# Kernel tuning notes

Hardware: AMD Instinct MI355X
Metric: run time of the kernel (lower is better)

## Reference

```python
import jax, jax.numpy as jnp
import numpy as np

B, S, D, H = 2, 2048, 1024, 16
DK = D // H  # 64


def setup_inputs() -> dict:
    key = jax.random.key(0)
    ks = jax.random.split(key, 12)
    inp = {
        "query": jax.random.normal(ks[0], (B, S, D), jnp.float32),
        "key": jax.random.normal(ks[1], (B, S, D), jnp.float32),
        "value": jax.random.normal(ks[2], (B, S, D), jnp.float32),
        "mask": jnp.ones((B, 1, S, S), jnp.float32),  # 1.0 = attend
    }
    sc = 1.0 / np.sqrt(D)
    inp["wq"] = jax.random.normal(ks[3], (D, D), jnp.float32) * sc
    inp["bq"] = jax.random.normal(ks[4], (D,), jnp.float32) * 0.01
    inp["wk"] = jax.random.normal(ks[5], (D, D), jnp.float32) * sc
    inp["bk"] = jax.random.normal(ks[6], (D,), jnp.float32) * 0.01
    inp["wv"] = jax.random.normal(ks[7], (D, D), jnp.float32) * sc
    inp["bv"] = jax.random.normal(ks[8], (D,), jnp.float32) * 0.01
    inp["wo"] = jax.random.normal(ks[9], (D, D), jnp.float32) * sc
    inp["bo"] = jax.random.normal(ks[10], (D,), jnp.float32) * 0.01
    return inp


def _split_heads(x):
    # [B, S, D] -> [B, H, S, DK]
    b, s, _ = x.shape
    return x.reshape(b, s, H, DK).transpose(0, 2, 1, 3)


def reference(query, key, value, mask, wq, bq, wk, bk, wv, bv, wo, bo):
    # Linear projections (torch Linear: x @ W.T + b)
    q = _split_heads(query @ wq.T + bq)   # [B,H,Sq,DK]
    k = _split_heads(key @ wk.T + bk)     # [B,H,Sk,DK]
    v = _split_heads(value @ wv.T + bv)   # [B,H,Sk,DK]

    attn = jnp.einsum('bhqd,bhkd->bhqk', q, k) / jnp.sqrt(jnp.float32(DK))
    # mask: 1.0 attend, 0.0 masked -> add finfo.min at masked positions
    inv = (1.0 - mask) * jnp.finfo(attn.dtype).min
    attn = attn + inv
    attention_weights = jax.nn.softmax(attn, axis=-1)  # [B,H,Sq,Sk]
    # dropout=0.0 (eval mode): identity
    ctx = jnp.einsum('bhqk,bhkd->bhqd', attention_weights, v)  # [B,H,Sq,DK]
    concat = ctx.transpose(0, 2, 1, 3).reshape(ctx.shape[0], ctx.shape[2], D)
    output = concat @ wo.T + bo
    return (output, attention_weights)
```

## Files before the change

kernel.cpp:

```cpp
#include <hip/hip_runtime.h>
#include <cstdint>

typedef short bf16x8 __attribute__((ext_vector_type(8)));
typedef float f32x4 __attribute__((ext_vector_type(4)));

#define NEG_MAX 3.402823466e38f

__device__ __forceinline__ unsigned short f2bf(float f) {
  uint32_t u = __builtin_bit_cast(uint32_t, f);
  u += 0x7FFFu + ((u >> 16) & 1u);
  return (unsigned short)(u >> 16);
}

__device__ __forceinline__ bf16x8 pack8(float4 x, float4 y) {
  bf16x8 r;
  r[0] = (short)f2bf(x.x); r[1] = (short)f2bf(x.y); r[2] = (short)f2bf(x.z); r[3] = (short)f2bf(x.w);
  r[4] = (short)f2bf(y.x); r[5] = (short)f2bf(y.y); r[6] = (short)f2bf(y.z); r[7] = (short)f2bf(y.w);
  return r;
}

__global__ __launch_bounds__(256) void cvt_w(const float* __restrict__ wq, const float* __restrict__ wk,
                                             const float* __restrict__ wv, const float* __restrict__ wo,
                                             unsigned short* __restrict__ out) {
  int i = blockIdx.x * 256 + threadIdx.x;
  const int sel = i >> 18;
  const int idx = i & 0x3FFFF;
  const float* src = (sel == 0) ? wq : (sel == 1) ? wk : (sel == 2) ? wv : wo;
  float4 v = reinterpret_cast<const float4*>(src)[idx];
  ushort4 o;
  o.x = f2bf(v.x); o.y = f2bf(v.y); o.z = f2bf(v.z); o.w = f2bf(v.w);
  reinterpret_cast<ushort4*>(out)[i] = o;
}

__global__ __launch_bounds__(256) void mask_scan(const float* __restrict__ mask,
                                                 int* __restrict__ flags) {
  const int blk = blockIdx.x;
  const int kt = blk & 31, qt = (blk >> 5) & 31, b = blk >> 10;
  const float* base = mask + ((size_t)b * 2048 + qt * 64) * 2048 + kt * 64;
  const int t = threadIdx.x;
  const int row = t >> 2, c0 = (t & 3) * 16;
  const float4* p = reinterpret_cast<const float4*>(base + (size_t)row * 2048 + c0);
  bool ones = true;
#pragma unroll
  for (int i = 0; i < 4; ++i) {
    float4 v = p[i];
    ones = ones && (v.x == 1.f) && (v.y == 1.f) && (v.z == 1.f) && (v.w == 1.f);
  }
  unsigned long long ball = __ballot(ones);
  __shared__ int sf[4];
  if ((t & 63) == 0) sf[t >> 6] = (ball == ~0ull) ? 1 : 0;
  __syncthreads();
  if (t == 0) flags[blk] = sf[0] & sf[1] & sf[2] & sf[3];
}

__global__ __launch_bounds__(256) void gemm_qkv(const float* __restrict__ Aq,
                                                const float* __restrict__ Ak,
                                                const float* __restrict__ Av,
                                                const unsigned short* __restrict__ W3,
                                                const float* __restrict__ bq,
                                                const float* __restrict__ bk,
                                                const float* __restrict__ bv,
                                                unsigned short* __restrict__ Qbf,
                                                unsigned short* __restrict__ Kbf,
                                                unsigned short* __restrict__ Vtb) {
  constexpr int KD = 1024;
  __shared__ __align__(16) unsigned short Al[128 * 32];
  __shared__ __align__(16) unsigned short Bl[128 * 32];
  const int tid = threadIdx.x;
  const int l = tid & 63;
  const int w = tid >> 6;
  const int lr = l & 15;
  const int lg = l >> 4;
  const int gm = blockIdx.y;
  const int gn = blockIdx.x;
  const int z = blockIdx.z;
  const int wr = w >> 1;
  const int wc = w & 1;

  const float* Af = (z == 0) ? Aq : (z == 1) ? Ak : Av;
  const float* bias = (z == 0) ? bq : (z == 1) ? bk : bv;
  const unsigned short* Bw = W3 + (size_t)z * 1048576;
  unsigned short* Cb = (z == 0) ? Qbf : (z == 1) ? Kbf : Vtb;

  f32x4 acc[4][4];
#pragma unroll
  for (int m = 0; m < 4; ++m)
#pragma unroll
    for (int n = 0; n < 4; ++n) acc[m][n] = (f32x4){0.f, 0.f, 0.f, 0.f};

  const int c0 = w * 2;
  const int srow = (l >> 2);
  const int scol = (l & 3) * 8;
  const unsigned short* gB = Bw + (size_t)(gn * 128) * KD;

  const int arow = tid >> 1;
  const int ahalf = tid & 1;
  const float* gA = Af + (size_t)(gm * 128 + arow) * KD + ahalf * 16;

  float4 ap[4];
  {
    const float4* p = reinterpret_cast<const float4*>(gA);
#pragma unroll
    for (int i = 0; i < 4; ++i) ap[i] = p[i];
  }

  for (int kt = 0; kt < 32; ++kt) {
    const int k0 = kt * 32;
    const unsigned short* b0 = gB + (size_t)(c0 * 16 + srow) * KD + k0 + scol;
    const unsigned short* b1 = b0 + (size_t)16 * KD;
    __builtin_amdgcn_global_load_lds((const __attribute__((address_space(1))) void*)b0,
                                     (__attribute__((address_space(3))) void*)&Bl[c0 * 512], 16, 0, 0);
    __builtin_amdgcn_global_load_lds((const __attribute__((address_space(1))) void*)b1,
                                     (__attribute__((address_space(3))) void*)&Bl[c0 * 512 + 512], 16, 0, 0);
    {
      bf16x8* dst = reinterpret_cast<bf16x8*>(&Al[arow * 32 + ahalf * 16]);
      dst[0] = pack8(ap[0], ap[1]);
      dst[1] = pack8(ap[2], ap[3]);
    }
    __syncthreads();
    if (kt + 1 < 32) {
      const float4* p = reinterpret_cast<const float4*>(gA + (kt + 1) * 32);
#pragma unroll
      for (int i = 0; i < 4; ++i) ap[i] = p[i];
    }
    bf16x8 af[4], bfr[4];
#pragma unroll
    for (int m = 0; m < 4; ++m)
      af[m] = *reinterpret_cast<const bf16x8*>(&Al[(wr * 64 + m * 16 + lr) * 32 + lg * 8]);
#pragma unroll
    for (int n = 0; n < 4; ++n)
      bfr[n] = *reinterpret_cast<const bf16x8*>(&Bl[(wc * 64 + n * 16 + lr) * 32 + lg * 8]);
#pragma unroll
    for (int m = 0; m < 4; ++m)
#pragma unroll
      for (int n = 0; n < 4; ++n)
        acc[m][n] = __builtin_amdgcn_mfma_f32_16x16x32_bf16(af[m], bfr[n], acc[m][n], 0, 0, 0);
    __syncthreads();
  }

#pragma unroll
  for (int m = 0; m < 4; ++m) {
#pragma unroll
    for (int n = 0; n < 4; ++n) {
      const int colg = gn * 128 + wc * 64 + n * 16 + lr;
      const float bv2 = bias[colg];
#pragma unroll
      for (int r = 0; r < 4; ++r) {
        const int rowg = gm * 128 + wr * 64 + m * 16 + lg * 4 + r;
        const float v = acc[m][n][r] + bv2;
        const int bb = rowg >> 11, ss = rowg & 2047;
        const int hh = colg >> 6, dk = colg & 63;
        if (z < 2)
          Cb[(((size_t)bb * 16 + hh) * 2048 + ss) * 64 + dk] = f2bf(v);
        else
          Cb[(((size_t)bb * 16 + hh) * 32 + (ss >> 6)) * 4096 + (size_t)dk * 64 + (ss & 63)] = f2bf(v);
      }
    }
  }
}

__global__ __launch_bounds__(256) void gemm_out(const unsigned short* __restrict__ A,
                                                const unsigned short* __restrict__ Bw,
                                                const float* __restrict__ bias,
                                                float* __restrict__ Cf) {
  constexpr int KD = 1024;
  __shared__ __align__(16) unsigned short Al[128 * 32];
  __shared__ __align__(16) unsigned short Bl[128 * 32];
  const int tid = threadIdx.x;
  const int l = tid & 63;
  const int w = tid >> 6;
  const int lr = l & 15;
  const int lg = l >> 4;
  const int gm = blockIdx.y;
  const int gn = blockIdx.x;
  const int wr = w >> 1;
  const int wc = w & 1;

  f32x4 acc[4][4];
#pragma unroll
  for (int m = 0; m < 4; ++m)
#pragma unroll
    for (int n = 0; n < 4; ++n) acc[m][n] = (f32x4){0.f, 0.f, 0.f, 0.f};

  const int c0 = w * 2;
  const int srow = (l >> 2);
  const int scol = (l & 3) * 8;
  const unsigned short* gA = A + (size_t)(gm * 128) * KD;
  const unsigned short* gB = Bw + (size_t)(gn * 128) * KD;

  for (int kt = 0; kt < 32; ++kt) {
    const int k0 = kt * 32;
    const unsigned short* a0 = gA + (size_t)(c0 * 16 + srow) * KD + k0 + scol;
    const unsigned short* a1 = a0 + (size_t)16 * KD;
    const unsigned short* b0 = gB + (size_t)(c0 * 16 + srow) * KD + k0 + scol;
    const unsigned short* b1 = b0 + (size_t)16 * KD;
    __builtin_amdgcn_global_load_lds((const __attribute__((address_space(1))) void*)a0,
                                     (__attribute__((address_space(3))) void*)&Al[c0 * 512], 16, 0, 0);
    __builtin_amdgcn_global_load_lds((const __attribute__((address_space(1))) void*)a1,
                                     (__attribute__((address_space(3))) void*)&Al[c0 * 512 + 512], 16, 0, 0);
    __builtin_amdgcn_global_load_lds((const __attribute__((address_space(1))) void*)b0,
                                     (__attribute__((address_space(3))) void*)&Bl[c0 * 512], 16, 0, 0);
    __builtin_amdgcn_global_load_lds((const __attribute__((address_space(1))) void*)b1,
                                     (__attribute__((address_space(3))) void*)&Bl[c0 * 512 + 512], 16, 0, 0);
    __syncthreads();
    bf16x8 af[4], bfr[4];
#pragma unroll
    for (int m = 0; m < 4; ++m)
      af[m] = *reinterpret_cast<const bf16x8*>(&Al[(wr * 64 + m * 16 + lr) * 32 + lg * 8]);
#pragma unroll
    for (int n = 0; n < 4; ++n)
      bfr[n] = *reinterpret_cast<const bf16x8*>(&Bl[(wc * 64 + n * 16 + lr) * 32 + lg * 8]);
#pragma unroll
    for (int m = 0; m < 4; ++m)
#pragma unroll
      for (int n = 0; n < 4; ++n)
        acc[m][n] = __builtin_amdgcn_mfma_f32_16x16x32_bf16(af[m], bfr[n], acc[m][n], 0, 0, 0);
    __syncthreads();
  }

#pragma unroll
  for (int m = 0; m < 4; ++m) {
#pragma unroll
    for (int n = 0; n < 4; ++n) {
      const int colg = gn * 128 + wc * 64 + n * 16 + lr;
      const float bv = bias[colg];
#pragma unroll
      for (int r = 0; r < 4; ++r) {
        const int rowg = gm * 128 + wr * 64 + m * 16 + lg * 4 + r;
        Cf[(size_t)rowg * 1024 + colg] = acc[m][n][r] + bv;
      }
    }
  }
}

__global__ __launch_bounds__(512, 4) void attn_fused(const unsigned short* __restrict__ Q,
                                                     const unsigned short* __restrict__ Kb,
                                                     const unsigned short* __restrict__ Vt,
                                                     const float* __restrict__ mask,
                                                     const int* __restrict__ flags,
                                                     float* __restrict__ wout,
                                                     unsigned short* __restrict__ ctx) {
  const int tid = threadIdx.x;
  const int l = tid & 63;
  const int w = tid >> 6;
  const int lr = l & 15;
  const int lg = l >> 4;

  const int d = blockIdx.x;
  const int bh = (d >> 7) * 8 + (d & 7);
  const int qp = (d >> 3) & 15;
  const int b = bh >> 4, h = bh & 15;
  const int q0 = qp * 128;

  __shared__ __align__(16) unsigned short KV[4][4096];
  __shared__ __align__(16) unsigned short Wl[8][16][64];

  const size_t qoff = ((size_t)bh * 2048 + (q0 + w * 16 + lr)) * 64 + lg * 8;
  const bf16x8 qf0 = *reinterpret_cast<const bf16x8*>(Q + qoff);
  const bf16x8 qf1 = *reinterpret_cast<const bf16x8*>(Q + qoff + 32);

  const int seg = tid;
  const int rs = seg >> 3, cx = (seg & 7) ^ (rs & 7);
  const unsigned short* kB = Kb + (size_t)bh * 131072;
  const unsigned short* vB = Vt + (size_t)bh * 131072;
  const size_t tS = (size_t)rs * 64 + cx * 8;
  const int ldsOff = w * 512;

  const int sA = (lg ^ (lr & 7)) << 3;
  const int sBo = ((4 + lg) ^ (lr & 7)) << 3;

  const int fbase = (b * 32 + qp * 2 + (w >> 2)) * 32;
  const uint32_t fmask = (uint32_t)__ballot(flags[fbase + (l & 31)] != 0);

  const float* mbase = mask + (size_t)b * 2048 * 2048;

#define STAGE(base_, kt_, slot_)                                                                       \
  do {                                                                                                 \
    __builtin_amdgcn_global_load_lds(                                                                  \
        (const __attribute__((address_space(1))) void*)((base_) + (size_t)(kt_) * 4096 + tS),          \
        (__attribute__((address_space(3))) void*)(&KV[slot_][0] + ldsOff), 16, 0, 0);                  \
  } while (0)

  float s0[4] = {0.f, 0.f, 0.f, 0.f};

  STAGE(kB, 0, 0);
  STAGE(kB, 1, 1);
  for (int kt = 0; kt < 32; ++kt) {
    if (kt < 31) {
      asm volatile("s_waitcnt vmcnt(1)" ::: "memory");
    } else {
      asm volatile("s_waitcnt vmcnt(0)" ::: "memory");
    }
    __builtin_amdgcn_s_barrier();
    __builtin_amdgcn_sched_barrier(0);
    const unsigned short* Ks = &KV[kt % 3][0];
    bf16x8 kf0[4], kf1[4];
#pragma unroll
    for (int n = 0; n < 4; ++n) {
      const int rb = (n * 16 + lr) * 64;
      kf0[n] = *reinterpret_cast<const bf16x8*>(&Ks[rb + sA]);
      kf1[n] = *reinterpret_cast<const bf16x8*>(&Ks[rb + sBo]);
    }
    if (kt + 2 < 32) STAGE(kB, kt + 2, (kt + 2) % 3);
    f32x4 acc[4];
#pragma unroll
    for (int n = 0; n < 4; ++n) {
      acc[n] = (f32x4){0.f, 0.f, 0.f, 0.f};
      acc[n] = __builtin_amdgcn_mfma_f32_16x16x32_bf16(qf0, kf0[n], acc[n], 0, 0, 0);
      acc[n] = __builtin_amdgcn_mfma_f32_16x16x32_bf16(qf1, kf1[n], acc[n], 0, 0, 0);
    }
    if ((fmask >> kt) & 1) {
#pragma unroll
      for (int r = 0; r < 4; ++r)
        s0[r] += __expf(acc[0][r] * 0.125f) + __expf(acc[1][r] * 0.125f) +
                 __expf(acc[2][r] * 0.125f) + __expf(acc[3][r] * 0.125f);
    } else {
#pragma unroll
      for (int r = 0; r < 4; ++r) {
        const int qrow = q0 + w * 16 + lg * 4 + r;
        const float* mp = mbase + (size_t)qrow * 2048 + kt * 64;
        float ps = 0.f;
#pragma unroll
        for (int n = 0; n < 4; ++n) {
          const float mv = mp[n * 16 + lr];
          ps += __expf(acc[n][r] * 0.125f + (1.0f - mv) * (-NEG_MAX));
        }
        s0[r] += ps;
      }
    }
  }

  float inv_s[4];
#pragma unroll
  for (int r = 0; r < 4; ++r) {
#pragma unroll
    for (int dd = 1; dd < 16; dd <<= 1) s0[r] += __shfl_xor(s0[r], dd);
    inv_s[r] = 1.0f / s0[r];
  }

  f32x4 cacc[4];
#pragma unroll
  for (int n = 0; n < 4; ++n) cacc[n] = (f32x4){0.f, 0.f, 0.f, 0.f};

  STAGE(kB, 0, 0);
  STAGE(vB, 0, 2);
  for (int kt = 0; kt < 32; ++kt) {
    const int cur = kt & 1;
    asm volatile("s_waitcnt vmcnt(0)" ::: "memory");
    __builtin_amdgcn_s_barrier();
    __builtin_amdgcn_sched_barrier(0);
    const unsigned short* Ks = &KV[cur][0];
    const unsigned short* Vs = &KV[2 + cur][0];
    bf16x8 kf0[4], kf1[4];
#pragma unroll
    for (int n = 0; n < 4; ++n) {
      const int rb = (n * 16 + lr) * 64;
      kf0[n] = *reinterpret_cast<const bf16x8*>(&Ks[rb + sA]);
      kf1[n] = *reinterpret_cast<const bf16x8*>(&Ks[rb + sBo]);
    }
    if (kt + 1 < 32) {
      STAGE(kB, kt + 1, cur ^ 1);
      STAGE(vB, kt + 1, 2 + (cur ^ 1));
    }
    f32x4 acc[4];
#pragma unroll
    for (int n = 0; n < 4; ++n) {
      acc[n] = (f32x4){0.f, 0.f, 0.f, 0.f};
      acc[n] = __builtin_amdgcn_mfma_f32_16x16x32_bf16(qf0, kf0[n], acc[n], 0, 0, 0);
      acc[n] = __builtin_amdgcn_mfma_f32_16x16x32_bf16(qf1, kf1[n], acc[n], 0, 0, 0);
    }
    const int fl = (fmask >> kt) & 1;
#pragma unroll
    for (int r = 0; r < 4; ++r) {
      const int qrow = q0 + w * 16 + lg * 4 + r;
      float* wp = wout + ((size_t)bh * 2048 + qrow) * 2048 + kt * 64;
      const int row2 = lg * 4 + r;
      const int rx = (row2 & 7) << 3;
      if (fl) {
#pragma unroll
        for (int n = 0; n < 4; ++n) {
          const float wgt = __expf(acc[n][r] * 0.125f) * inv_s[r];
          __builtin_nontemporal_store(wgt, &wp[n * 16 + lr]);
          Wl[w][row2][(n * 16 + lr) ^ rx] = f2bf(wgt);
        }
      } else {
        const float* mp = mbase + (size_t)qrow * 2048 + kt * 64;
#pragma unroll
        for (int n = 0; n < 4; ++n) {
          const float mv = mp[n * 16 + lr];
          const float wgt = __expf(acc[n][r] * 0.125f + (1.0f - mv) * (-NEG_MAX)) * inv_s[r];
          __builtin_nontemporal_store(wgt, &wp[n * 16 + lr]);
          Wl[w][row2][(n * 16 + lr) ^ rx] = f2bf(wgt);
        }
      }
    }
    bf16x8 vf0[4], vf1[4];
#pragma unroll
    for (int n = 0; n < 4; ++n) {
      const int rb = (n * 16 + lr) * 64;
      vf0[n] = *reinterpret_cast<const bf16x8*>(&Vs[rb + sA]);
      vf1[n] = *reinterpret_cast<const bf16x8*>(&Vs[rb + sBo]);
    }
    asm volatile("s_waitcnt lgkmcnt(0)" ::: "memory");
    __builtin_amdgcn_sched_barrier(0);
    const bf16x8 a0 = *reinterpret_cast<const bf16x8*>(&Wl[w][lr][(lg ^ (lr & 7)) * 8]);
    const bf16x8 a1 = *reinterpret_cast<const bf16x8*>(&Wl[w][lr][((4 | lg) ^ (lr & 7)) * 8]);
#pragma unroll
    for (int n = 0; n < 4; ++n) {
      cacc[n] = __builtin_amdgcn_mfma_f32_16x16x32_bf16(a0, vf0[n], cacc[n], 0, 0, 0);
      cacc[n] = __builtin_amdgcn_mfma_f32_16x16x32_bf16(a1, vf1[n], cacc[n], 0, 0, 0);
    }
  }

#pragma unroll
  for (int n = 0; n < 4; ++n) {
#pragma unroll
    for (int r = 0; r < 4; ++r) {
      const int ss = q0 + w * 16 + lg * 4 + r;
      const int col = h * 64 + n * 16 + lr;
      ctx[((size_t)b * 2048 + ss) * 1024 + col] = f2bf(cacc[n][r]);
    }
  }
#undef STAGE
}

extern "C" void kernel_launch(void* const* d_in, const int* in_sizes, int n_in,
                              void* d_out, int out_size, void* d_ws, size_t ws_size,
                              hipStream_t stream) {
  const float* query = (const float*)d_in[0];
  const float* key   = (const float*)d_in[1];
  const float* value = (const float*)d_in[2];
  const float* mask  = (const float*)d_in[3];
  const float* wq = (const float*)d_in[4];
  const float* bq = (const float*)d_in[5];
  const float* wk = (const float*)d_in[6];
  const float* bk = (const float*)d_in[7];
  const float* wv = (const float*)d_in[8];
  const float* bv = (const float*)d_in[9];
  const float* wo = (const float*)d_in[10];
  const float* bo = (const float*)d_in[11];

  unsigned short* Qbf = (unsigned short*)d_ws;
  unsigned short* Kbf = Qbf + 4194304;
  unsigned short* Vtb = Kbf + 4194304;
  unsigned short* ctx = Vtb + 4194304;
  unsigned short* wbf4 = ctx + 4194304;
  int* flags = (int*)(wbf4 + 4194304);

  float* outp = (float*)d_out;
  float* wout = outp + 4194304;

  mask_scan<<<2048, 256, 0, stream>>>(mask, flags);
  cvt_w<<<4096, 256, 0, stream>>>(wq, wk, wv, wo, wbf4);

  dim3 gq(8, 32, 3);
  gemm_qkv<<<gq, 256, 0, stream>>>(query, key, value, wbf4, bq, bk, bv, Qbf, Kbf, Vtb);

  attn_fused<<<512, 512, 0, stream>>>(Qbf, Kbf, Vtb, mask, flags, wout, ctx);

  dim3 gg(8, 32);
  gemm_out<<<gg, 256, 0, stream>>>(ctx, wbf4 + 3145728, bo, outp);
}
```

Before: 309.2 us.

## Stage attention weights through LDS for vectorized coalesced stores, use exp2

The attention-weight output was written as scattered scalar fp32 stores from the MFMA register layout. It is now written by reading back the bf16 copy already held in LDS, expanding it to fp32, and issuing four 16-byte nontemporal vector stores per lane, so each lane writes contiguous row segments. Because the values come from the bf16 copy, the returned attention weights now carry only bf16 precision. The unmasked softmax path uses exp2f with a folded log2e scale instead of __expf. The loop-top wait becomes vmcnt(4), so the four outstanding stores no longer block the K/V prefetch wait.

```diff
diff --git a/kernel.cpp b/kernel.cpp
--- a/kernel.cpp
+++ b/kernel.cpp
@@ -5,11 +5,16 @@
 typedef float f32x4 __attribute__((ext_vector_type(4)));
 
 #define NEG_MAX 3.402823466e38f
+#define C_EXP2 0.1803368801111244f
 
 __device__ __forceinline__ unsigned short f2bf(float f) {
   uint32_t u = __builtin_bit_cast(uint32_t, f);
   u += 0x7FFFu + ((u >> 16) & 1u);
   return (unsigned short)(u >> 16);
+}
+
+__device__ __forceinline__ float bf2f(unsigned short s) {
+  return __builtin_bit_cast(float, (uint32_t)s << 16);
 }
 
 __device__ __forceinline__ bf16x8 pack8(float4 x, float4 y) {
@@ -274,6 +279,12 @@
 
   const float* mbase = mask + (size_t)b * 2048 * 2048;
 
+  const int wrow = l >> 2;
+  const int c0w = (l & 3) * 16;
+  const int rxw = (wrow & 7) << 3;
+  const int rb1 = (c0w ^ (rxw & 48)) + (rxw & 8);
+  const int rb2 = (c0w ^ (rxw & 48)) + (8 ^ (rxw & 8));
+
 #define STAGE(base_, kt_, slot_)                                                                       \
   do {                                                                                                 \
     __builtin_amdgcn_global_load_lds(                                                                  \
@@ -312,8 +323,8 @@
     if ((fmask >> kt) & 1) {
 #pragma unroll
       for (int r = 0; r < 4; ++r)
-        s0[r] += __expf(acc[0][r] * 0.125f) + __expf(acc[1][r] * 0.125f) +
-                 __expf(acc[2][r] * 0.125f) + __expf(acc[3][r] * 0.125f);
+        s0[r] += exp2f(acc[0][r] * C_EXP2) + exp2f(acc[1][r] * C_EXP2) +
+                 exp2f(acc[2][r] * C_EXP2) + exp2f(acc[3][r] * C_EXP2);
     } else {
 #pragma unroll
       for (int r = 0; r < 4; ++r) {
@@ -346,7 +357,11 @@
   STAGE(vB, 0, 2);
   for (int kt = 0; kt < 32; ++kt) {
     const int cur = kt & 1;
-    asm volatile("s_waitcnt vmcnt(0)" ::: "memory");
+    if (kt == 0) {
+      asm volatile("s_waitcnt vmcnt(0)" ::: "memory");
+    } else {
+      asm volatile("s_waitcnt vmcnt(4)" ::: "memory");
+    }
     __builtin_amdgcn_s_barrier();
     __builtin_amdgcn_sched_barrier(0);
     const unsigned short* Ks = &KV[cur][0];
@@ -372,24 +387,21 @@
     const int fl = (fmask >> kt) & 1;
 #pragma unroll
     for (int r = 0; r < 4; ++r) {
-      const int qrow = q0 + w * 16 + lg * 4 + r;
-      float* wp = wout + ((size_t)bh * 2048 + qrow) * 2048 + kt * 64;
       const int row2 = lg * 4 + r;
       const int rx = (row2 & 7) << 3;
       if (fl) {
 #pragma unroll
         for (int n = 0; n < 4; ++n) {
-          const float wgt = __expf(acc[n][r] * 0.125f) * inv_s[r];
-          __builtin_nontemporal_store(wgt, &wp[n * 16 + lr]);
+          const float wgt = exp2f(acc[n][r] * C_EXP2) * inv_s[r];
           Wl[w][row2][(n * 16 + lr) ^ rx] = f2bf(wgt);
         }
       } else {
+        const int qrow = q0 + w * 16 + row2;
         const float* mp = mbase + (size_t)qrow * 2048 + kt * 64;
 #pragma unroll
         for (int n = 0; n < 4; ++n) {
           const float mv = mp[n * 16 + lr];
           const float wgt = __expf(acc[n][r] * 0.125f + (1.0f - mv) * (-NEG_MAX)) * inv_s[r];
-          __builtin_nontemporal_store(wgt, &wp[n * 16 + lr]);
           Wl[w][row2][(n * 16 + lr) ^ rx] = f2bf(wgt);
         }
       }
@@ -403,6 +415,25 @@
     }
     asm volatile("s_waitcnt lgkmcnt(0)" ::: "memory");
     __builtin_amdgcn_sched_barrier(0);
+    {
+      const bf16x8 wb1 = *reinterpret_cast<const bf16x8*>(&Wl[w][wrow][rb1]);
+      const bf16x8 wb2 = *reinterpret_cast<const bf16x8*>(&Wl[w][wrow][rb2]);
+      f32x4 f0, f1, f2, f3;
+      f0[0] = bf2f((unsigned short)wb1[0]); f0[1] = bf2f((unsigned short)wb1[1]);
+      f0[2] = bf2f((unsigned short)wb1[2]); f0[3] = bf2f((unsigned short)wb1[3]);
+      f1[0] = bf2f((unsigned short)wb1[4]); f1[1] = bf2f((unsigned short)wb1[5]);
+      f1[2] = bf2f((unsigned short)wb1[6]); f1[3] = bf2f((unsigned short)wb1[7]);
+      f2[0] = bf2f((unsigned short)wb2[0]); f2[1] = bf2f((unsigned short)wb2[1]);
+      f2[2] = bf2f((unsigned short)wb2[2]); f2[3] = bf2f((unsigned short)wb2[3]);
+      f3[0] = bf2f((unsigned short)wb2[4]); f3[1] = bf2f((unsigned short)wb2[5]);
+      f3[2] = bf2f((unsigned short)wb2[6]); f3[3] = bf2f((unsigned short)wb2[7]);
+      f32x4* wpv = reinterpret_cast<f32x4*>(
+          wout + ((size_t)bh * 2048 + q0 + w * 16 + wrow) * 2048 + kt * 64 + c0w);
+      __builtin_nontemporal_store(f0, wpv);
+      __builtin_nontemporal_store(f1, wpv + 1);
+      __builtin_nontemporal_store(f2, wpv + 2);
+      __builtin_nontemporal_store(f3, wpv + 3);
+    }
     const bf16x8 a0 = *reinterpret_cast<const bf16x8*>(&Wl[w][lr][(lg ^ (lr & 7)) * 8]);
     const bf16x8 a1 = *reinterpret_cast<const bf16x8*>(&Wl[w][lr][((4 | lg) ^ (lr & 7)) * 8]);
 #pragma unroll
```

Result: slower. 947.7 us (+206.5%).
